# Kernel tuning notes

Measured on AMD Instinct MI355X. Metric: run time of the kernel, lower is better.

## Reference

```python
import jax, jax.numpy as jnp
import numpy as np

LN_EPS = 1e-5

def setup_inputs() -> dict:
    key = jax.random.key(0)
    ks = jax.random.split(key, 10)
    L, B, D, C, O = 512, 2, 256, 128, 64
    s_in = 1.0 / np.sqrt(D)
    s_ch = 1.0 / np.sqrt(C)
    return {
        "x": jax.random.normal(ks[0], (L, B, D), dtype=jnp.float32),
        "ln_gamma": jnp.ones((D,), dtype=jnp.float32),
        "ln_beta": jnp.zeros((D,), dtype=jnp.float32),
        "w1": jax.random.uniform(ks[1], (D, C), jnp.float32, -s_in, s_in),
        "b1": jax.random.uniform(ks[2], (C,), jnp.float32, -s_in, s_in),
        "w2": jax.random.uniform(ks[3], (D, C), jnp.float32, -s_in, s_in),
        "b2": jax.random.uniform(ks[4], (C,), jnp.float32, -s_in, s_in),
        "w3": jax.random.uniform(ks[5], (C, O), jnp.float32, -s_ch, s_ch),
        "b3": jax.random.uniform(ks[6], (O,), jnp.float32, -s_ch, s_ch),
        "w4": jax.random.uniform(ks[7], (C, O), jnp.float32, -s_ch, s_ch),
    }

def _layernorm(x, gamma, beta):
    mu = jnp.mean(x, axis=-1, keepdims=True)
    var = jnp.mean(jnp.square(x - mu), axis=-1, keepdims=True)
    return (x - mu) * jax.lax.rsqrt(var + LN_EPS) * gamma + beta

def reference(x, ln_gamma, ln_beta, w1, b1, w2, b2, w3, b3, w4):
    # x: (L, B, D) -> (B, L, D)
    xb = jnp.transpose(x, (1, 0, 2))
    xb = _layernorm(xb, ln_gamma, ln_beta)
    a = xb @ w1 + b1  # (B, L, C)
    b = xb @ w2 + b2  # (B, L, C)
    # (a_l * b_m) @ w3  -> contract channel dim directly into output channels
    mul_term = jnp.einsum('blc,bmc,co->blmo', a, b, w3) + b3
    # (a_l - b_m) @ w4  -> distribute linearity to avoid (B,L,L,C) materialization
    a4 = a @ w4  # (B, L, O)
    b4 = b @ w4  # (B, L, O)
    sub_term = a4[:, :, None, :] - b4[:, None, :, :]
    return mul_term + sub_term  # (B, L, L, O)
```

## Files before the change

kernel.cpp:

```cpp
#include <hip/hip_runtime.h>
#include <hip/hip_bf16.h>

#define LL 512
#define BB 2
#define DD 256
#define CC 128
#define OO 64

typedef __attribute__((ext_vector_type(8))) short bf16x8;
typedef __attribute__((ext_vector_type(4))) float f32x4;

__device__ __forceinline__ short f2bf(float v) {
    __hip_bfloat16 h = __float2bfloat16(v);
    return *reinterpret_cast<short*>(&h);
}

__device__ __forceinline__ float wave_reduce_sum(float v) {
#pragma unroll
    for (int off = 32; off > 0; off >>= 1)
        v += __shfl_down(v, off, 64);
    return v;
}

__global__ __launch_bounds__(256) void prep_kernel(
    const float* __restrict__ x,
    const float* __restrict__ gamma,
    const float* __restrict__ beta,
    const float* __restrict__ w1, const float* __restrict__ b1,
    const float* __restrict__ w2, const float* __restrict__ b2,
    const float* __restrict__ w4, const float* __restrict__ b3,
    const float* __restrict__ w3,
    float* __restrict__ a_ws, __hip_bfloat16* __restrict__ bact,
    float* __restrict__ a4b3_ws,
    float* __restrict__ w3t_ws, float* __restrict__ w4t_ws)
{
    const int blk = blockIdx.x;
    const int b = blk >> 9;
    const int l = blk & (LL - 1);
    const int t = threadIdx.x;

    __shared__ float ylds[DD];
    __shared__ float ashare[CC];
    __shared__ float red[8];

    {
        const int idx = blk * 256 + t;
        if (idx < 2 * CC * OO) {
            const float* src = (idx < CC * OO) ? w3 : w4;
            float* dst = (idx < CC * OO) ? w3t_ws : w4t_ws;
            const int i = idx & (CC * OO - 1);
            const int o = i & (OO - 1);
            const int c = i >> 6;
            dst[o * CC + c] = src[i];
        }
    }

    float xv = x[(l * BB + b) * DD + t];
    float s = wave_reduce_sum(xv);
    if ((t & 63) == 0) red[t >> 6] = s;
    __syncthreads();
    float mu = (red[0] + red[1] + red[2] + red[3]) * (1.0f / DD);
    float xc = xv - mu;
    float s2 = wave_reduce_sum(xc * xc);
    if ((t & 63) == 0) red[4 + (t >> 6)] = s2;
    __syncthreads();
    float var = (red[4] + red[5] + red[6] + red[7]) * (1.0f / DD);
    float y = xc * rsqrtf(var + 1e-5f) * gamma[t] + beta[t];
    ylds[t] = y;
    __syncthreads();

    {
        const int c = t & (CC - 1);
        const float* w = (t < CC) ? w1 : w2;
        float acc = (t < CC) ? b1[c] : b2[c];
#pragma unroll 16
        for (int d = 0; d < DD; ++d)
            acc = fmaf(ylds[d], w[d * CC + c], acc);
        if (t < CC) {
            a_ws[(b * LL + l) * CC + c] = acc;
            ashare[c] = acc;
        } else {
            bact[(b * LL + l) * CC + c] = __float2bfloat16(acc);
        }
    }
    __syncthreads();

    if (t < OO) {
        float acc = b3[t];
#pragma unroll 16
        for (int c = 0; c < CC; ++c)
            acc = fmaf(ashare[c], w4[c * OO + t], acc);
        a4b3_ws[(b * LL + l) * OO + t] = acc;
    }
}

__global__ __launch_bounds__(256, 4) void main_kernel(
    const float* __restrict__ a_ws, const __hip_bfloat16* __restrict__ bact,
    const float* __restrict__ a4b3_ws,
    const float* __restrict__ w3t, const float* __restrict__ w4t,
    float* __restrict__ out)
{
    const int bid = blockIdx.x;
    const int mh = bid & 1;
    const int l  = (bid >> 1) & (LL - 1);
    const int b  = bid >> 10;
    const int t  = threadIdx.x;
    const int wave = t >> 6;
    const int lane = t & 63;
    const int ln = lane & 15;
    const int q  = lane >> 4;

    __shared__ alignas(16) unsigned short Wt[OO * CC];
    __shared__ float stile[4][16 * 68];

    const float* arow = a_ws + (b * LL + l) * CC;
    {
        const int g  = t & 15;
        const int orr = t >> 4;
        const int c0 = g * 8;
        const float4 a0 = *(const float4*)(arow + c0);
        const float4 a1 = *(const float4*)(arow + c0 + 4);
#pragma unroll
        for (int i = 0; i < 4; ++i) {
            const int o = i * 16 + orr;
            const float* p3 = w3t + o * CC + c0;
            const float* p4 = w4t + o * CC + c0;
            const float4 x0 = *(const float4*)(p3);
            const float4 x1 = *(const float4*)(p3 + 4);
            const float4 y0 = *(const float4*)(p4);
            const float4 y1 = *(const float4*)(p4 + 4);
            bf16x8 v;
            v[0] = f2bf(fmaf(a0.x, x0.x, -y0.x));
            v[1] = f2bf(fmaf(a0.y, x0.y, -y0.y));
            v[2] = f2bf(fmaf(a0.z, x0.z, -y0.z));
            v[3] = f2bf(fmaf(a0.w, x0.w, -y0.w));
            v[4] = f2bf(fmaf(a1.x, x1.x, -y1.x));
            v[5] = f2bf(fmaf(a1.y, x1.y, -y1.y));
            v[6] = f2bf(fmaf(a1.z, x1.z, -y1.z));
            v[7] = f2bf(fmaf(a1.w, x1.w, -y1.w));
            *(bf16x8*)(&Wt[o * CC + ((g ^ (o & 15)) * 8)]) = v;
        }
    }

    const int mbase = mh * 256 + wave * 64;
    const short* abase = (const short*)bact + ((size_t)(b * LL + mbase + ln)) * CC + q * 8;

    float a4v[4];
    const float* a4p = a4b3_ws + (b * LL + l) * OO;
#pragma unroll
    for (int ot = 0; ot < 4; ++ot)
        a4v[ot] = a4p[ot * 16 + ln];

    f32x4 acc[4][4];
#pragma unroll
    for (int mt = 0; mt < 4; ++mt)
#pragma unroll
        for (int ot = 0; ot < 4; ++ot)
            acc[mt][ot] = (f32x4){0.f, 0.f, 0.f, 0.f};

    __syncthreads();

#pragma unroll
    for (int ks = 0; ks < 4; ++ks) {
        bf16x8 af[4], bfr[4];
#pragma unroll
        for (int mt = 0; mt < 4; ++mt)
            af[mt] = *(const bf16x8*)(abase + mt * (16 * CC) + ks * 32);
#pragma unroll
        for (int ot = 0; ot < 4; ++ot) {
            const int o = ot * 16 + ln;
            const int gr = (ks * 4 + q) ^ ln;
            bfr[ot] = *(const bf16x8*)(&Wt[o * CC + gr * 8]);
        }
#pragma unroll
        for (int mt = 0; mt < 4; ++mt)
#pragma unroll
            for (int ot = 0; ot < 4; ++ot)
                acc[mt][ot] = __builtin_amdgcn_mfma_f32_16x16x32_bf16(
                    af[mt], bfr[ot], acc[mt][ot], 0, 0, 0);
    }

    float* outbase = out + (((size_t)(b * LL + l)) * LL + mbase) * OO;
    float* sw = stile[wave];
#pragma unroll
    for (int mt = 0; mt < 4; ++mt) {
#pragma unroll
        for (int ot = 0; ot < 4; ++ot)
#pragma unroll
            for (int r = 0; r < 4; ++r)
                sw[(q * 4 + r) * 68 + ot * 16 + ln] = acc[mt][ot][r] + a4v[ot];
#pragma unroll
        for (int i = 0; i < 4; ++i) {
            const int idx = i * 64 + lane;
            const int row = idx >> 4;
            const int col = (idx & 15) * 4;
            const float4 v = *(const float4*)(sw + row * 68 + col);
            *(float4*)(outbase + (mt * 16 + row) * OO + col) = v;
        }
    }
}

extern "C" void kernel_launch(void* const* d_in, const int* in_sizes, int n_in,
                              void* d_out, int out_size, void* d_ws, size_t ws_size,
                              hipStream_t stream) {
    const float* x     = (const float*)d_in[0];
    const float* gamma = (const float*)d_in[1];
    const float* beta  = (const float*)d_in[2];
    const float* w1    = (const float*)d_in[3];
    const float* b1    = (const float*)d_in[4];
    const float* w2    = (const float*)d_in[5];
    const float* b2    = (const float*)d_in[6];
    const float* w3    = (const float*)d_in[7];
    const float* b3    = (const float*)d_in[8];
    const float* w4    = (const float*)d_in[9];
    float* out = (float*)d_out;

    char* ws = (char*)d_ws;
    float* a_ws            = (float*)ws;
    __hip_bfloat16* bact   = (__hip_bfloat16*)(ws + 512*1024);
    float* a4b3_ws         = (float*)(ws + 768*1024);
    float* w3t_ws          = (float*)(ws + 1024*1024);
    float* w4t_ws          = (float*)(ws + 1024*1024 + 32*1024);

    prep_kernel<<<BB * LL, 256, 0, stream>>>(x, gamma, beta, w1, b1, w2, b2,
                                             w4, b3, w3,
                                             a_ws, bact, a4b3_ws, w3t_ws, w4t_ws);
    main_kernel<<<BB * LL * 2, 256, 0, stream>>>(a_ws, bact, a4b3_ws,
                                                 w3t_ws, w4t_ws, out);
}
```

Measured before the change: 176.6 us.

## Precompute per-row bf16 combined weight in prep kernel, drop LDS staging in main

The prep kernel now builds, for each (b,l) row, the bf16 matrix a_l*w3 - w4 already laid out in MFMA fragment order and writes it to workspace (16 KB per row, 16 MB total). The main kernel reads B-fragments straight from global memory, with no LDS weight tile, no in-block conversion and no barrier. Each combined matrix is built once instead of twice (once per m-half block), but this adds a 16 MB write plus reread. The new path is taken only if the workspace is large enough; otherwise the old path is kept.

```diff
diff --git a/kernel.cpp b/kernel.cpp
--- a/kernel.cpp
+++ b/kernel.cpp
@@ -20,6 +20,155 @@
     for (int off = 32; off > 0; off >>= 1)
         v += __shfl_down(v, off, 64);
     return v;
+}
+
+__global__ __launch_bounds__(256) void prep_fused(
+    const float* __restrict__ x,
+    const float* __restrict__ gamma,
+    const float* __restrict__ beta,
+    const float* __restrict__ w1, const float* __restrict__ b1,
+    const float* __restrict__ w2, const float* __restrict__ b2,
+    const float* __restrict__ w3, const float* __restrict__ b3,
+    const float* __restrict__ w4,
+    __hip_bfloat16* __restrict__ bact, float* __restrict__ a4b3_ws,
+    short* __restrict__ wt_ws)
+{
+    const int blk = blockIdx.x;
+    const int b = blk >> 9;
+    const int l = blk & (LL - 1);
+    const int t = threadIdx.x;
+
+    __shared__ float ylds[DD];
+    __shared__ float ashare[CC];
+    __shared__ float red[8];
+
+    float xv = x[(l * BB + b) * DD + t];
+    float s = wave_reduce_sum(xv);
+    if ((t & 63) == 0) red[t >> 6] = s;
+    __syncthreads();
+    float mu = (red[0] + red[1] + red[2] + red[3]) * (1.0f / DD);
+    float xc = xv - mu;
+    float s2 = wave_reduce_sum(xc * xc);
+    if ((t & 63) == 0) red[4 + (t >> 6)] = s2;
+    __syncthreads();
+    float var = (red[4] + red[5] + red[6] + red[7]) * (1.0f / DD);
+    float y = xc * rsqrtf(var + 1e-5f) * gamma[t] + beta[t];
+    ylds[t] = y;
+    __syncthreads();
+
+    {
+        const int c = t & (CC - 1);
+        const float* w = (t < CC) ? w1 : w2;
+        float acc = (t < CC) ? b1[c] : b2[c];
+#pragma unroll 16
+        for (int d = 0; d < DD; ++d)
+            acc = fmaf(ylds[d], w[d * CC + c], acc);
+        if (t < CC) {
+            ashare[c] = acc;
+        } else {
+            bact[(b * LL + l) * CC + c] = __float2bfloat16(acc);
+        }
+    }
+    __syncthreads();
+
+    if (t < OO) {
+        float acc = b3[t];
+#pragma unroll 16
+        for (int c = 0; c < CC; ++c)
+            acc = fmaf(ashare[c], w4[c * OO + t], acc);
+        a4b3_ws[(b * LL + l) * OO + t] = acc;
+    }
+
+    {
+        const int q = t >> 6;
+        const int o = t & 63;
+        short* dstb = wt_ws + (size_t)blk * 8192;
+#pragma unroll
+        for (int ks = 0; ks < 4; ++ks) {
+            const int cbase = ks * 32 + q * 8;
+            bf16x8 v;
+#pragma unroll
+            for (int j = 0; j < 8; ++j) {
+                const int c = cbase + j;
+                v[j] = f2bf(fmaf(ashare[c], w3[c * OO + o], -w4[c * OO + o]));
+            }
+            *(bf16x8*)(dstb + (size_t)(ks * 256 + t) * 8) = v;
+        }
+    }
+}
+
+__global__ __launch_bounds__(256, 4) void main_fused(
+    const __hip_bfloat16* __restrict__ bact,
+    const float* __restrict__ a4b3_ws,
+    const short* __restrict__ wt_ws,
+    float* __restrict__ out)
+{
+    const int bid = blockIdx.x;
+    const int mh = bid & 1;
+    const int l  = (bid >> 1) & (LL - 1);
+    const int b  = bid >> 10;
+    const int t  = threadIdx.x;
+    const int wave = t >> 6;
+    const int lane = t & 63;
+    const int ln = lane & 15;
+    const int q  = lane >> 4;
+
+    __shared__ float stile[4][16 * 68];
+
+    const int mbase = mh * 256 + wave * 64;
+    const short* abase = (const short*)bact
+        + ((size_t)(b * LL + mbase + ln)) * CC + q * 8;
+    const short* wtb = wt_ws + ((size_t)(b * LL + l)) * 8192;
+
+    float a4v[4];
+    const float* a4p = a4b3_ws + (b * LL + l) * OO;
+#pragma unroll
+    for (int ot = 0; ot < 4; ++ot)
+        a4v[ot] = a4p[ot * 16 + ln];
+
+    f32x4 acc[4][4];
+#pragma unroll
+    for (int mt = 0; mt < 4; ++mt)
+#pragma unroll
+        for (int ot = 0; ot < 4; ++ot)
+            acc[mt][ot] = (f32x4){0.f, 0.f, 0.f, 0.f};
+
+#pragma unroll
+    for (int ks = 0; ks < 4; ++ks) {
+        bf16x8 af[4], bfr[4];
+#pragma unroll
+        for (int mt = 0; mt < 4; ++mt)
+            af[mt] = *(const bf16x8*)(abase + mt * (16 * CC) + ks * 32);
+#pragma unroll
+        for (int ot = 0; ot < 4; ++ot)
+            bfr[ot] = *(const bf16x8*)(wtb
+                + (size_t)((((ks * 4 + q) * 4 + ot) * 16 + ln) * 8));
+#pragma unroll
+        for (int mt = 0; mt < 4; ++mt)
+#pragma unroll
+            for (int ot = 0; ot < 4; ++ot)
+                acc[mt][ot] = __builtin_amdgcn_mfma_f32_16x16x32_bf16(
+                    af[mt], bfr[ot], acc[mt][ot], 0, 0, 0);
+    }
+
+    float* outbase = out + (((size_t)(b * LL + l)) * LL + mbase) * OO;
+    float* sw = stile[wave];
+#pragma unroll
+    for (int mt = 0; mt < 4; ++mt) {
+#pragma unroll
+        for (int ot = 0; ot < 4; ++ot)
+#pragma unroll
+            for (int r = 0; r < 4; ++r)
+                sw[(q * 4 + r) * 68 + ot * 16 + ln] = acc[mt][ot][r] + a4v[ot];
+#pragma unroll
+        for (int i = 0; i < 4; ++i) {
+            const int idx = i * 64 + lane;
+            const int row = idx >> 4;
+            const int col = (idx & 15) * 4;
+            const float4 v = *(const float4*)(sw + row * 68 + col);
+            *(float4*)(outbase + (mt * 16 + row) * OO + col) = v;
+        }
+    }
 }
 
 __global__ __launch_bounds__(256) void prep_kernel(
@@ -216,15 +365,25 @@
     float* out = (float*)d_out;
 
     char* ws = (char*)d_ws;
-    float* a_ws            = (float*)ws;
-    __hip_bfloat16* bact   = (__hip_bfloat16*)(ws + 512*1024);
-    float* a4b3_ws         = (float*)(ws + 768*1024);
-    float* w3t_ws          = (float*)(ws + 1024*1024);
-    float* w4t_ws          = (float*)(ws + 1024*1024 + 32*1024);
-
-    prep_kernel<<<BB * LL, 256, 0, stream>>>(x, gamma, beta, w1, b1, w2, b2,
-                                             w4, b3, w3,
-                                             a_ws, bact, a4b3_ws, w3t_ws, w4t_ws);
-    main_kernel<<<BB * LL * 2, 256, 0, stream>>>(a_ws, bact, a4b3_ws,
-                                                 w3t_ws, w4t_ws, out);
-}
+    const size_t need_fused = 512 * 1024 + (size_t)BB * LL * 8192 * sizeof(short);
+
+    if (ws_size >= need_fused) {
+        __hip_bfloat16* bact = (__hip_bfloat16*)ws;
+        float* a4b3_ws       = (float*)(ws + 256 * 1024);
+        short* wt_ws         = (short*)(ws + 512 * 1024);
+        prep_fused<<<BB * LL, 256, 0, stream>>>(x, gamma, beta, w1, b1, w2, b2,
+                                                w3, b3, w4, bact, a4b3_ws, wt_ws);
+        main_fused<<<BB * LL * 2, 256, 0, stream>>>(bact, a4b3_ws, wt_ws, out);
+    } else {
+        float* a_ws            = (float*)ws;
+        __hip_bfloat16* bact   = (__hip_bfloat16*)(ws + 512*1024);
+        float* a4b3_ws         = (float*)(ws + 768*1024);
+        float* w3t_ws          = (float*)(ws + 1024*1024);
+        float* w4t_ws          = (float*)(ws + 1024*1024 + 32*1024);
+        prep_kernel<<<BB * LL, 256, 0, stream>>>(x, gamma, beta, w1, b1, w2, b2,
+                                                 w4, b3, w3,
+                                                 a_ws, bact, a4b3_ws, w3t_ws, w4t_ws);
+        main_kernel<<<BB * LL * 2, 256, 0, stream>>>(a_ws, bact, a4b3_ws,
+                                                     w3t_ws, w4t_ws, out);
+    }
+}
```

Result: slower. 190.0 us (+7.6%).
